# Kernel optimization log

Hardware: AMD Instinct MI355X
Metric: run time of the kernel (lower is better)

## Reference

```python
import jax, jax.numpy as jnp
import numpy as np

D_IN = 768
D_OUT = 768
NUM_HEADS = 12
HEAD_DIM = D_OUT // NUM_HEADS


def setup_inputs() -> dict:
    key = jax.random.key(0)
    ks = jax.random.split(key, 6)
    s = 1.0 / np.sqrt(D_IN)
    X = jax.random.normal(ks[0], (4, 2048, D_IN), dtype=jnp.float32)
    Wq = jax.random.uniform(ks[1], (D_IN, D_OUT), jnp.float32, -s, s)
    Wk = jax.random.uniform(ks[2], (D_IN, D_OUT), jnp.float32, -s, s)
    Wv = jax.random.uniform(ks[3], (D_IN, D_OUT), jnp.float32, -s, s)
    Wo = jax.random.uniform(ks[4], (D_OUT, D_OUT), jnp.float32, -s, s)
    bo = jax.random.uniform(ks[5], (D_OUT,), jnp.float32, -s, s)
    return {"X": X, "Wq": Wq, "Wk": Wk, "Wv": Wv, "Wo": Wo, "bo": bo}


def reference(X, Wq, Wk, Wv, Wo, bo):
    b, n, _ = X.shape
    # QKV projections, split heads -> [b, h, n, d]
    def split(t):
        return t.reshape(b, n, NUM_HEADS, HEAD_DIM).transpose(0, 2, 1, 3)
    q = split(X @ Wq)
    k = split(X @ Wk)
    v = split(X @ Wv)
    scores = jnp.einsum('bhqd,bhkd->bhqk', q, k) / np.sqrt(HEAD_DIM).astype(np.float32)
    causal = jnp.triu(jnp.ones((n, n), dtype=bool), k=1)
    scores = jnp.where(causal, -jnp.inf, scores)
    attn = jax.nn.softmax(scores, axis=-1)  # dropout p=0 -> identity
    ctx = jnp.einsum('bhqk,bhkd->bhqd', attn, v)
    ctx = ctx.transpose(0, 2, 1, 3).reshape(b, n, D_OUT)
    return ctx @ Wo + bo
```

## Files before the change

### kernel.cpp

```cpp
#include <hip/hip_runtime.h>
#include <stdint.h>

#define B_  4
#define N_  2048
#define D_  768
#define H_  12
#define HD_ 64
#define M_  (B_*N_)

typedef short bf8 __attribute__((ext_vector_type(8)));
typedef float f32x4 __attribute__((ext_vector_type(4)));

static __device__ __forceinline__ unsigned short f2bf(float f) {
    unsigned u = __float_as_uint(f);
    unsigned r = u + 0x7fffu + ((u >> 16) & 1u);
    return (unsigned short)(r >> 16);
}

#define GLOAD_LDS16(gptr, lptr)                                                   \
    __builtin_amdgcn_global_load_lds(                                             \
        (const __attribute__((address_space(1))) void*)(gptr),                    \
        (__attribute__((address_space(3))) void*)(lptr), 16, 0, 0)

__global__ __launch_bounds__(256) void convert_x(const float* __restrict__ X,
                                                 unsigned short* __restrict__ Xb) {
    const size_t i = ((size_t)blockIdx.x * 256 + threadIdx.x) * 8;
    const float4 a = *(const float4*)(X + i);
    const float4 b = *(const float4*)(X + i + 4);
    ushort4 lo, hi;
    lo.x = f2bf(a.x); lo.y = f2bf(a.y); lo.z = f2bf(a.z); lo.w = f2bf(a.w);
    hi.x = f2bf(b.x); hi.y = f2bf(b.y); hi.z = f2bf(b.z); hi.w = f2bf(b.w);
    *(ushort4*)(Xb + i)     = lo;
    *(ushort4*)(Xb + i + 4) = hi;
}

__global__ __launch_bounds__(256) void transpose_w(
    const float* __restrict__ Wq, const float* __restrict__ Wk,
    const float* __restrict__ Wv, const float* __restrict__ Wo,
    unsigned short* __restrict__ Wqt, unsigned short* __restrict__ Wkt,
    unsigned short* __restrict__ Wvt, unsigned short* __restrict__ Wot)
{
    __shared__ float tile[32][33];
    const int z = blockIdx.z;
    const float* W = (z == 0) ? Wq : (z == 1) ? Wk : (z == 2) ? Wv : Wo;
    unsigned short* Wt = (z == 0) ? Wqt : (z == 1) ? Wkt : (z == 2) ? Wvt : Wot;
    const int k0 = blockIdx.x * 32, n0 = blockIdx.y * 32;
    const int tx = threadIdx.x & 31, ty = threadIdx.x >> 5;
    #pragma unroll
    for (int i = 0; i < 4; ++i)
        tile[ty + 8 * i][tx] = W[(size_t)(k0 + ty + 8 * i) * D_ + n0 + tx];
    __syncthreads();
    #pragma unroll
    for (int i = 0; i < 4; ++i)
        Wt[(size_t)(n0 + ty + 8 * i) * D_ + k0 + tx] = f2bf(tile[tx][ty + 8 * i]);
}

__global__ __launch_bounds__(256) void qkv_mfma(
    const unsigned short* __restrict__ Xb,
    const unsigned short* __restrict__ Wqt, const unsigned short* __restrict__ Wkt,
    const unsigned short* __restrict__ Wvt,
    unsigned short* __restrict__ Qb, unsigned short* __restrict__ Kb,
    unsigned short* __restrict__ Vt)
{
    __shared__ unsigned short As[128 * 32];
    __shared__ unsigned short Bs[128 * 32];

    const int t = threadIdx.x;
    const int wave = t >> 6, lane = t & 63;
    const int col = lane & 15, quad = lane >> 4;
    const int wm = (wave & 1) * 64, wn = (wave >> 1) * 64;

    const int m0 = blockIdx.x * 128;
    const int n0 = blockIdx.y * 128;
    const int mat = blockIdx.z;
    const unsigned short* Wt = (mat == 0) ? Wqt : (mat == 1) ? Wkt : Wvt;

    const unsigned short* Ag0 = Xb + (size_t)(m0 + (t >> 2)) * D_ + (t & 3) * 8;
    const unsigned short* Ag1 = Ag0 + (size_t)64 * D_;
    const unsigned short* Bg0 = Wt + (size_t)(n0 + (t >> 2)) * D_ + (t & 3) * 8;
    const unsigned short* Bg1 = Bg0 + (size_t)64 * D_;
    unsigned short* AsW0 = As + wave * 512;
    unsigned short* AsW1 = As + 2048 + wave * 512;
    unsigned short* BsW0 = Bs + wave * 512;
    unsigned short* BsW1 = Bs + 2048 + wave * 512;

    f32x4 acc[4][4] = {};

    for (int k0 = 0; k0 < D_; k0 += 32) {
        __syncthreads();
        GLOAD_LDS16(Ag0 + k0, AsW0);
        GLOAD_LDS16(Ag1 + k0, AsW1);
        GLOAD_LDS16(Bg0 + k0, BsW0);
        GLOAD_LDS16(Bg1 + k0, BsW1);
        __syncthreads();

        bf8 a[4], b[4];
        #pragma unroll
        for (int i = 0; i < 4; ++i)
            a[i] = *(const bf8*)(As + (wm + i * 16 + col) * 32 + quad * 8);
        #pragma unroll
        for (int j = 0; j < 4; ++j)
            b[j] = *(const bf8*)(Bs + (wn + j * 16 + col) * 32 + quad * 8);
        #pragma unroll
        for (int i = 0; i < 4; ++i)
            #pragma unroll
            for (int j = 0; j < 4; ++j)
                acc[i][j] = __builtin_amdgcn_mfma_f32_16x16x32_bf16(a[i], b[j], acc[i][j], 0, 0, 0);
    }

    if (mat != 2) {
        unsigned short* Out = (mat == 0) ? Qb : Kb;
        #pragma unroll
        for (int j = 0; j < 4; ++j) {
            const int n = n0 + wn + j * 16 + col;
            const int h = n >> 6, d = n & 63;
            #pragma unroll
            for (int i = 0; i < 4; ++i) {
                const int mb = m0 + wm + i * 16 + quad * 4;
                const int bb = mb >> 11, nn = mb & (N_ - 1);
                unsigned short* op = Out + ((size_t)(bb * H_ + h) * N_ + nn) * HD_ + d;
                #pragma unroll
                for (int r = 0; r < 4; ++r) op[(size_t)r * HD_] = f2bf(acc[i][j][r]);
            }
        }
    } else {
        #pragma unroll
        for (int j = 0; j < 4; ++j) {
            const int n = n0 + wn + j * 16 + col;
            const int h = n >> 6, d = n & 63;
            #pragma unroll
            for (int i = 0; i < 4; ++i) {
                const int mb = m0 + wm + i * 16 + quad * 4;
                const int bb = mb >> 11, nn = mb & (N_ - 1);
                ushort4 pk;
                pk.x = f2bf(acc[i][j][0]); pk.y = f2bf(acc[i][j][1]);
                pk.z = f2bf(acc[i][j][2]); pk.w = f2bf(acc[i][j][3]);
                *(ushort4*)(Vt + ((size_t)(bb * H_ + h) * HD_ + d) * N_ + nn) = pk;
            }
        }
    }
}

#define PS 72

static __device__ __forceinline__ void qk_softmax(
    const bf8 (&ka)[4][2], bf8 qb0, bf8 qb1,
    int k0, int q, bool mask,
    float& mrun, float& lrun, float& alpha,
    unsigned short* Pw, int col, int quad)
{
    f32x4 s[4] = {};
    #pragma unroll
    for (int kc = 0; kc < 4; ++kc) {
        s[kc] = __builtin_amdgcn_mfma_f32_16x16x32_bf16(ka[kc][0], qb0, s[kc], 0, 0, 0);
        s[kc] = __builtin_amdgcn_mfma_f32_16x16x32_bf16(ka[kc][1], qb1, s[kc], 0, 0, 0);
    }
    float sv[4][4];
    if (mask) {
        #pragma unroll
        for (int kc = 0; kc < 4; ++kc)
            #pragma unroll
            for (int r = 0; r < 4; ++r) {
                const int key = k0 + kc * 16 + quad * 4 + r;
                sv[kc][r] = (key > q) ? -INFINITY : s[kc][r] * 0.125f;
            }
    } else {
        #pragma unroll
        for (int kc = 0; kc < 4; ++kc)
            #pragma unroll
            for (int r = 0; r < 4; ++r) sv[kc][r] = s[kc][r] * 0.125f;
    }

    float mt = sv[0][0];
    #pragma unroll
    for (int kc = 0; kc < 4; ++kc)
        #pragma unroll
        for (int r = 0; r < 4; ++r) mt = fmaxf(mt, sv[kc][r]);
    mt = fmaxf(mt, __shfl_xor(mt, 16, 64));
    mt = fmaxf(mt, __shfl_xor(mt, 32, 64));

    const float mnew = fmaxf(mrun, mt);
    alpha = __expf(mrun - mnew);
    mrun = mnew;

    float p[4][4], psum = 0.f;
    #pragma unroll
    for (int kc = 0; kc < 4; ++kc)
        #pragma unroll
        for (int r = 0; r < 4; ++r) {
            p[kc][r] = __expf(sv[kc][r] - mnew);
            psum += p[kc][r];
        }
    psum += __shfl_xor(psum, 16, 64);
    psum += __shfl_xor(psum, 32, 64);
    lrun = lrun * alpha + psum;

    #pragma unroll
    for (int kc = 0; kc < 4; ++kc) {
        ushort4 pk;
        pk.x = f2bf(p[kc][0]); pk.y = f2bf(p[kc][1]);
        pk.z = f2bf(p[kc][2]); pk.w = f2bf(p[kc][3]);
        *(ushort4*)(Pw + col * PS + kc * 16 + quad * 4) = pk;
    }
}

static __device__ __forceinline__ void pv_acc(
    const unsigned short* Pw, const bf8 (&va)[4][2],
    float alpha, f32x4 (&o)[4], int col, int quad)
{
    const bf8 pb0 = *(const bf8*)(Pw + col * PS + quad * 8);
    const bf8 pb1 = *(const bf8*)(Pw + col * PS + 32 + quad * 8);
    #pragma unroll
    for (int dc = 0; dc < 4; ++dc)
        #pragma unroll
        for (int r = 0; r < 4; ++r) o[dc][r] *= alpha;
    #pragma unroll
    for (int dc = 0; dc < 4; ++dc) {
        o[dc] = __builtin_amdgcn_mfma_f32_16x16x32_bf16(va[dc][0], pb0, o[dc], 0, 0, 0);
        o[dc] = __builtin_amdgcn_mfma_f32_16x16x32_bf16(va[dc][1], pb1, o[dc], 0, 0, 0);
    }
}

__global__ __launch_bounds__(256, 3) void attn_mfma(
    const unsigned short* __restrict__ Qb,
    const unsigned short* __restrict__ Kb,
    const unsigned short* __restrict__ Vt,
    unsigned short* __restrict__ Ctxb)
{
    __shared__ unsigned short Kl[64 * PS];
    __shared__ unsigned short Vl[64 * PS];
    __shared__ unsigned short Pl[4][2][16 * PS];

    const int t = threadIdx.x;
    const int wave = t >> 6;
    const int lane = t & 63;
    const int col  = lane & 15;
    const int quad = lane >> 4;

    const int bid = blockIdx.x;
    const int bh  = bid >> 4;
    const int x   = bid & 15;
    const int tl  = x, th = 31 - x;
    const int q0L = tl * 64 + wave * 16;
    const int q0H = th * 64 + wave * 16;
    const int qL  = q0L + col;
    const int qH  = q0H + col;

    const unsigned short* Kp = Kb + (size_t)bh * N_ * HD_;
    const unsigned short* Vp = Vt + (size_t)bh * HD_ * N_;
    const unsigned short* QpL = Qb + ((size_t)bh * N_ + q0L) * HD_;
    const unsigned short* QpH = Qb + ((size_t)bh * N_ + q0H) * HD_;

    const bf8 qbL0 = *(const bf8*)(QpL + (size_t)col * HD_ + quad * 8);
    const bf8 qbL1 = *(const bf8*)(QpL + (size_t)col * HD_ + 32 + quad * 8);
    const bf8 qbH0 = *(const bf8*)(QpH + (size_t)col * HD_ + quad * 8);
    const bf8 qbH1 = *(const bf8*)(QpH + (size_t)col * HD_ + 32 + quad * 8);

    f32x4 oL[4] = {}, oH[4] = {};
    float mL = -INFINITY, lL = 0.f, mH = -INFINITY, lH = 0.f;

    unsigned short* PwH = &Pl[wave][0][0];
    unsigned short* PwL = &Pl[wave][1][0];

    const int srow = t >> 3;
    const int scol = (t & 7) * 8;
    const unsigned short* Kg = Kp + (size_t)srow * HD_ + scol;
    const unsigned short* Vg = Vp + (size_t)srow * N_ + scol;
    unsigned short* KlD0 = Kl + srow * PS + scol;
    unsigned short* KlD1 = Kl + (srow + 32) * PS + scol;
    unsigned short* VlD0 = Vl + srow * PS + scol;
    unsigned short* VlD1 = Vl + (srow + 32) * PS + scol;

    uint4 kr0 = *(const uint4*)(Kg);
    uint4 kr1 = *(const uint4*)(Kg + (size_t)32 * HD_);
    uint4 vr0 = *(const uint4*)(Vg);
    uint4 vr1 = *(const uint4*)(Vg + (size_t)32 * N_);

    const int iters = 32 - x;
    for (int kt = 0; kt < iters; ++kt) {
        const int k0 = kt * 64;
        const bool actL = (kt <= tl);

        *(uint4*)KlD0 = kr0;
        *(uint4*)KlD1 = kr1;
        *(uint4*)VlD0 = vr0;
        *(uint4*)VlD1 = vr1;
        __syncthreads();

        if (kt + 1 < iters) {
            const size_t k1 = (size_t)(k0 + 64);
            kr0 = *(const uint4*)(Kg + k1 * HD_);
            kr1 = *(const uint4*)(Kg + (k1 + 32) * HD_);
            vr0 = *(const uint4*)(Vg + k1);
            vr1 = *(const uint4*)(Vg + (size_t)32 * N_ + k1);
        }

        bf8 ka[4][2];
        #pragma unroll
        for (int kc = 0; kc < 4; ++kc) {
            ka[kc][0] = *(const bf8*)(Kl + (kc * 16 + col) * PS + quad * 8);
            ka[kc][1] = *(const bf8*)(Kl + (kc * 16 + col) * PS + 32 + quad * 8);
        }

        float aH, aL;
        qk_softmax(ka, qbH0, qbH1, k0, qH, kt == th, mH, lH, aH, PwH, col, quad);
        if (actL)
            qk_softmax(ka, qbL0, qbL1, k0, qL, kt == tl, mL, lL, aL, PwL, col, quad);

        bf8 va[4][2];
        #pragma unroll
        for (int dc = 0; dc < 4; ++dc) {
            va[dc][0] = *(const bf8*)(Vl + (dc * 16 + col) * PS + quad * 8);
            va[dc][1] = *(const bf8*)(Vl + (dc * 16 + col) * PS + 32 + quad * 8);
        }

        pv_acc(PwH, va, aH, oH, col, quad);
        if (actL)
            pv_acc(PwL, va, aL, oL, col, quad);

        __syncthreads();
    }

    const int b = bh / H_;
    const int h = bh % H_;
    {
        const float inv = 1.0f / lH;
        unsigned short* cp = Ctxb + ((size_t)(b * N_ + qH)) * D_ + h * HD_;
        #pragma unroll
        for (int dc = 0; dc < 4; ++dc) {
            ushort4 pk;
            pk.x = f2bf(oH[dc][0] * inv); pk.y = f2bf(oH[dc][1] * inv);
            pk.z = f2bf(oH[dc][2] * inv); pk.w = f2bf(oH[dc][3] * inv);
            *(ushort4*)(cp + dc * 16 + quad * 4) = pk;
        }
    }
    {
        const float inv = 1.0f / lL;
        unsigned short* cp = Ctxb + ((size_t)(b * N_ + qL)) * D_ + h * HD_;
        #pragma unroll
        for (int dc = 0; dc < 4; ++dc) {
            ushort4 pk;
            pk.x = f2bf(oL[dc][0] * inv); pk.y = f2bf(oL[dc][1] * inv);
            pk.z = f2bf(oL[dc][2] * inv); pk.w = f2bf(oL[dc][3] * inv);
            *(ushort4*)(cp + dc * 16 + quad * 4) = pk;
        }
    }
}

__global__ __launch_bounds__(256) void out_mfma(
    const unsigned short* __restrict__ Ctxb,
    const unsigned short* __restrict__ Wot,
    const float* __restrict__ bo,
    float* __restrict__ Out)
{
    __shared__ unsigned short As[128 * 32];
    __shared__ unsigned short Bs[128 * 32];

    const int t = threadIdx.x;
    const int wave = t >> 6, lane = t & 63;
    const int col = lane & 15, quad = lane >> 4;
    const int wm = (wave & 1) * 64, wn = (wave >> 1) * 64;

    const int m0 = blockIdx.x * 128;
    const int n0 = blockIdx.y * 128;

    const unsigned short* Ag0 = Ctxb + (size_t)(m0 + (t >> 2)) * D_ + (t & 3) * 8;
    const unsigned short* Ag1 = Ag0 + (size_t)64 * D_;
    const unsigned short* Bg0 = Wot + (size_t)(n0 + (t >> 2)) * D_ + (t & 3) * 8;
    const unsigned short* Bg1 = Bg0 + (size_t)64 * D_;
    unsigned short* AsW0 = As + wave * 512;
    unsigned short* AsW1 = As + 2048 + wave * 512;
    unsigned short* BsW0 = Bs + wave * 512;
    unsigned short* BsW1 = Bs + 2048 + wave * 512;

    f32x4 acc[4][4] = {};

    for (int k0 = 0; k0 < D_; k0 += 32) {
        __syncthreads();
        GLOAD_LDS16(Ag0 + k0, AsW0);
        GLOAD_LDS16(Ag1 + k0, AsW1);
        GLOAD_LDS16(Bg0 + k0, BsW0);
        GLOAD_LDS16(Bg1 + k0, BsW1);
        __syncthreads();

        bf8 a[4], b[4];
        #pragma unroll
        for (int i = 0; i < 4; ++i)
            a[i] = *(const bf8*)(As + (wm + i * 16 + col) * 32 + quad * 8);
        #pragma unroll
        for (int j = 0; j < 4; ++j)
            b[j] = *(const bf8*)(Bs + (wn + j * 16 + col) * 32 + quad * 8);
        #pragma unroll
        for (int i = 0; i < 4; ++i)
            #pragma unroll
            for (int j = 0; j < 4; ++j)
                acc[i][j] = __builtin_amdgcn_mfma_f32_16x16x32_bf16(a[i], b[j], acc[i][j], 0, 0, 0);
    }

    #pragma unroll
    for (int j = 0; j < 4; ++j) {
        const int n = n0 + wn + j * 16 + col;
        const float bias = bo[n];
        #pragma unroll
        for (int i = 0; i < 4; ++i) {
            const int mb = m0 + wm + i * 16 + quad * 4;
            #pragma unroll
            for (int r = 0; r < 4; ++r)
                Out[(size_t)(mb + r) * D_ + n] = acc[i][j][r] + bias;
        }
    }
}

extern "C" void kernel_launch(void* const* d_in, const int* in_sizes, int n_in,
                              void* d_out, int out_size, void* d_ws, size_t ws_size,
                              hipStream_t stream) {
    const float* X  = (const float*)d_in[0];
    const float* Wq = (const float*)d_in[1];
    const float* Wk = (const float*)d_in[2];
    const float* Wv = (const float*)d_in[3];
    const float* Wo = (const float*)d_in[4];
    const float* bo = (const float*)d_in[5];
    float* out = (float*)d_out;

    const size_t elems = (size_t)M_ * D_;
    const size_t welems = (size_t)D_ * D_;
    unsigned short* Xb  = (unsigned short*)d_ws;
    unsigned short* Wqt = Xb + elems;
    unsigned short* Wkt = Wqt + welems;
    unsigned short* Wvt = Wkt + welems;
    unsigned short* Wot = Wvt + welems;
    unsigned short* Qb  = Wot + welems;
    unsigned short* Kb  = Qb + elems;
    unsigned short* Vt  = Kb + elems;
    unsigned short* Ctxb = Xb;

    convert_x<<<dim3(elems / 2048), 256, 0, stream>>>(X, Xb);
    transpose_w<<<dim3(24, 24, 4), 256, 0, stream>>>(Wq, Wk, Wv, Wo, Wqt, Wkt, Wvt, Wot);

    qkv_mfma<<<dim3(M_ / 128, D_ / 128, 3), 256, 0, stream>>>(Xb, Wqt, Wkt, Wvt, Qb, Kb, Vt);

    attn_mfma<<<dim3(B_ * H_ * 16), 256, 0, stream>>>(Qb, Kb, Vt, Ctxb);

    out_mfma<<<dim3(M_ / 128, D_ / 128), 256, 0, stream>>>(Ctxb, Wot, bo, out);
}
```

Measured before the change: 227.3 us.

## Fold softmax scale into Q, use exp2 with lazy rescale, share P buffer

New measurement: 221.8 us. 2.5% less time.

```diff
diff --git a/kernel.cpp b/kernel.cpp
--- a/kernel.cpp
+++ b/kernel.cpp
@@ -17,10 +17,23 @@
     return (unsigned short)(r >> 16);
 }
 
+static __device__ __forceinline__ unsigned pk2bf(float f0, float f1) {
+    return ((__float_as_uint(f1) + 0x8000u) & 0xFFFF0000u) |
+           ((__float_as_uint(f0) + 0x8000u) >> 16);
+}
+
+#if __has_builtin(__builtin_amdgcn_exp2f)
+#define EXP2(x) __builtin_amdgcn_exp2f(x)
+#else
+#define EXP2(x) exp2f(x)
+#endif
+
 #define GLOAD_LDS16(gptr, lptr)                                                   \
     __builtin_amdgcn_global_load_lds(                                             \
         (const __attribute__((address_space(1))) void*)(gptr),                    \
         (__attribute__((address_space(3))) void*)(lptr), 16, 0, 0)
+
+#define QSCALE 0.1803368801111204f
 
 __global__ __launch_bounds__(256) void convert_x(const float* __restrict__ X,
                                                  unsigned short* __restrict__ Xb) {
@@ -110,6 +123,7 @@
 
     if (mat != 2) {
         unsigned short* Out = (mat == 0) ? Qb : Kb;
+        const float qsc = (mat == 0) ? QSCALE : 1.0f;
         #pragma unroll
         for (int j = 0; j < 4; ++j) {
             const int n = n0 + wn + j * 16 + col;
@@ -120,7 +134,7 @@
                 const int bb = mb >> 11, nn = mb & (N_ - 1);
                 unsigned short* op = Out + ((size_t)(bb * H_ + h) * N_ + nn) * HD_ + d;
                 #pragma unroll
-                for (int r = 0; r < 4; ++r) op[(size_t)r * HD_] = f2bf(acc[i][j][r]);
+                for (int r = 0; r < 4; ++r) op[(size_t)r * HD_] = f2bf(acc[i][j][r] * qsc);
             }
         }
     } else {
@@ -146,7 +160,7 @@
 static __device__ __forceinline__ void qk_softmax(
     const bf8 (&ka)[4][2], bf8 qb0, bf8 qb1,
     int k0, int q, bool mask,
-    float& mrun, float& lrun, float& alpha,
+    float& mrun, float& lrun, f32x4 (&o)[4],
     unsigned short* Pw, int col, int quad)
 {
     f32x4 s[4] = {};
@@ -162,13 +176,13 @@
             #pragma unroll
             for (int r = 0; r < 4; ++r) {
                 const int key = k0 + kc * 16 + quad * 4 + r;
-                sv[kc][r] = (key > q) ? -INFINITY : s[kc][r] * 0.125f;
+                sv[kc][r] = (key > q) ? -INFINITY : s[kc][r];
             }
     } else {
         #pragma unroll
         for (int kc = 0; kc < 4; ++kc)
             #pragma unroll
-            for (int r = 0; r < 4; ++r) sv[kc][r] = s[kc][r] * 0.125f;
+            for (int r = 0; r < 4; ++r) sv[kc][r] = s[kc][r];
     }
 
     float mt = sv[0][0];
@@ -179,41 +193,44 @@
     mt = fmaxf(mt, __shfl_xor(mt, 16, 64));
     mt = fmaxf(mt, __shfl_xor(mt, 32, 64));
 
-    const float mnew = fmaxf(mrun, mt);
-    alpha = __expf(mrun - mnew);
-    mrun = mnew;
+    if (__any(mt > mrun)) {
+        const float mnew = fmaxf(mrun, mt);
+        const float al   = EXP2(mrun - mnew);
+        mrun = mnew;
+        lrun *= al;
+        #pragma unroll
+        for (int dc = 0; dc < 4; ++dc)
+            #pragma unroll
+            for (int r = 0; r < 4; ++r) o[dc][r] *= al;
+    }
 
     float p[4][4], psum = 0.f;
     #pragma unroll
     for (int kc = 0; kc < 4; ++kc)
         #pragma unroll
         for (int r = 0; r < 4; ++r) {
-            p[kc][r] = __expf(sv[kc][r] - mnew);
+            p[kc][r] = EXP2(sv[kc][r] - mrun);
             psum += p[kc][r];
         }
     psum += __shfl_xor(psum, 16, 64);
     psum += __shfl_xor(psum, 32, 64);
-    lrun = lrun * alpha + psum;
+    lrun += psum;
 
     #pragma unroll
     for (int kc = 0; kc < 4; ++kc) {
-        ushort4 pk;
-        pk.x = f2bf(p[kc][0]); pk.y = f2bf(p[kc][1]);
-        pk.z = f2bf(p[kc][2]); pk.w = f2bf(p[kc][3]);
-        *(ushort4*)(Pw + col * PS + kc * 16 + quad * 4) = pk;
+        uint2 pk;
+        pk.x = pk2bf(p[kc][0], p[kc][1]);
+        pk.y = pk2bf(p[kc][2], p[kc][3]);
+        *(uint2*)(Pw + col * PS + kc * 16 + quad * 4) = pk;
     }
 }
 
 static __device__ __forceinline__ void pv_acc(
     const unsigned short* Pw, const bf8 (&va)[4][2],
-    float alpha, f32x4 (&o)[4], int col, int quad)
+    f32x4 (&o)[4], int col, int quad)
 {
     const bf8 pb0 = *(const bf8*)(Pw + col * PS + quad * 8);
     const bf8 pb1 = *(const bf8*)(Pw + col * PS + 32 + quad * 8);
-    #pragma unroll
-    for (int dc = 0; dc < 4; ++dc)
-        #pragma unroll
-        for (int r = 0; r < 4; ++r) o[dc][r] *= alpha;
     #pragma unroll
     for (int dc = 0; dc < 4; ++dc) {
         o[dc] = __builtin_amdgcn_mfma_f32_16x16x32_bf16(va[dc][0], pb0, o[dc], 0, 0, 0);
@@ -229,7 +246,7 @@
 {
     __shared__ unsigned short Kl[64 * PS];
     __shared__ unsigned short Vl[64 * PS];
-    __shared__ unsigned short Pl[4][2][16 * PS];
+    __shared__ unsigned short Pl[4][16 * PS];
 
     const int t = threadIdx.x;
     const int wave = t >> 6;
@@ -259,8 +276,7 @@
     f32x4 oL[4] = {}, oH[4] = {};
     float mL = -INFINITY, lL = 0.f, mH = -INFINITY, lH = 0.f;
 
-    unsigned short* PwH = &Pl[wave][0][0];
-    unsigned short* PwL = &Pl[wave][1][0];
+    unsigned short* Pw = &Pl[wave][0];
 
     const int srow = t >> 3;
     const int scol = (t & 7) * 8;
@@ -302,10 +318,7 @@
             ka[kc][1] = *(const bf8*)(Kl + (kc * 16 + col) * PS + 32 + quad * 8);
         }
 
-        float aH, aL;
-        qk_softmax(ka, qbH0, qbH1, k0, qH, kt == th, mH, lH, aH, PwH, col, quad);
-        if (actL)
-            qk_softmax(ka, qbL0, qbL1, k0, qL, kt == tl, mL, lL, aL, PwL, col, quad);
+        qk_softmax(ka, qbH0, qbH1, k0, qH, kt == th, mH, lH, oH, Pw, col, quad);
 
         bf8 va[4][2];
         #pragma unroll
@@ -314,9 +327,12 @@
             va[dc][1] = *(const bf8*)(Vl + (dc * 16 + col) * PS + 32 + quad * 8);
         }
 
-        pv_acc(PwH, va, aH, oH, col, quad);
-        if (actL)
-            pv_acc(PwL, va, aL, oL, col, quad);
+        pv_acc(Pw, va, oH, col, quad);
+
+        if (actL) {
+            qk_softmax(ka, qbL0, qbL1, k0, qL, kt == tl, mL, lL, oL, Pw, col, quad);
+            pv_acc(Pw, va, oL, col, quad);
+        }
 
         __syncthreads();
     }
@@ -328,10 +344,10 @@
         unsigned short* cp = Ctxb + ((size_t)(b * N_ + qH)) * D_ + h * HD_;
         #pragma unroll
         for (int dc = 0; dc < 4; ++dc) {
-            ushort4 pk;
-            pk.x = f2bf(oH[dc][0] * inv); pk.y = f2bf(oH[dc][1] * inv);
-            pk.z = f2bf(oH[dc][2] * inv); pk.w = f2bf(oH[dc][3] * inv);
-            *(ushort4*)(cp + dc * 16 + quad * 4) = pk;
+            uint2 pk;
+            pk.x = pk2bf(oH[dc][0] * inv, oH[dc][1] * inv);
+            pk.y = pk2bf(oH[dc][2] * inv, oH[dc][3] * inv);
+            *(uint2*)(cp + dc * 16 + quad * 4) = pk;
         }
     }
     {
@@ -339,10 +355,10 @@
         unsigned short* cp = Ctxb + ((size_t)(b * N_ + qL)) * D_ + h * HD_;
         #pragma unroll
         for (int dc = 0; dc < 4; ++dc) {
-            ushort4 pk;
-            pk.x = f2bf(oL[dc][0] * inv); pk.y = f2bf(oL[dc][1] * inv);
-            pk.z = f2bf(oL[dc][2] * inv); pk.w = f2bf(oL[dc][3] * inv);
-            *(ushort4*)(cp + dc * 16 + quad * 4) = pk;
+            uint2 pk;
+            pk.x = pk2bf(oL[dc][0] * inv, oL[dc][1] * inv);
+            pk.y = pk2bf(oL[dc][2] * inv, oL[dc][3] * inv);
+            *(uint2*)(cp + dc * 16 + quad * 4) = pk;
         }
     }
 }
```
